# Optimization experiments

Measured on AMD Instinct MI355X. Metric: run time of the kernel, lower is better.

Reference implementation:

```python
import jax, jax.numpy as jnp
import numpy as np


def setup_inputs() -> dict:
    key = jax.random.key(0)
    k1, k2, k3, k4 = jax.random.split(key, 4)
    n, b, h, f = 8, 64, 128, 256
    hs = 64
    x = jax.random.normal(k1, (n, b, h, f), dtype=jnp.float32)
    # torch Linear weights are (out, in); store transposed as (in, out) for x @ W
    Wq = jax.random.normal(k2, (f, hs), dtype=jnp.float32) * (6.0 / (f + hs)) ** 0.5
    Wk = jax.random.normal(k3, (f, hs), dtype=jnp.float32) * (6.0 / (f + hs)) ** 0.5
    Wv = jax.random.normal(k4, (f, hs), dtype=jnp.float32) * (6.0 / (f + hs)) ** 0.5
    return {"x": x, "Wq": Wq, "Wk": Wk, "Wv": Wv}


def reference(x, Wq, Wk, Wv):
    # x: (n, b, h, f). NOTE: scale uses f = n_embd (as in the source), not head_size.
    f = x.shape[-1]
    scale = f ** (-0.5)
    Q = jnp.einsum('nbhf,fd->nbhd', x, Wq)  # (n, b, h, hs)
    K = jnp.einsum('nbhf,fd->nbhd', x, Wk)
    V = jnp.einsum('nbhf,fd->nbhd', x, Wv)
    # alphas[i, j, b, p, q] = sum_d Q[j,b,p,d] * K[i,b,q,d] * scale
    scores = jnp.einsum('jbpd,ibqd->ijbpq', Q, K) * scale  # (n, n, b, h, h)
    alphas = jax.nn.softmax(scores, axis=-1)
    # out[i, j, b, p, d] = sum_q alphas[i,j,b,p,q] V[i,b,q,d]; then sum over i
    o = jnp.einsum('ijbpq,ibqd->jbpd', alphas, V)  # (n, b, h, hs)
    return o
```

## Files before the change

### kernel.cpp

```cpp
#include <hip/hip_runtime.h>
#include <cstdint>

#define N_SEQ 8
#define B_DIM 64
#define H_DIM 128
#define F_DIM 256
#define HS 64

typedef __attribute__((ext_vector_type(8))) short short8;
typedef __attribute__((ext_vector_type(4))) float floatx4;

__device__ __forceinline__ ushort f2bf(float f) {
    union { float f; uint32_t u; } v; v.f = f;
    uint32_t r = v.u + 0x7FFF + ((v.u >> 16) & 1);
    return (ushort)(r >> 16);
}

__device__ __forceinline__ void async_ld16(const ushort* g, ushort* lds) {
    __builtin_amdgcn_global_load_lds(
        (const __attribute__((address_space(1))) unsigned int*)g,
        (__attribute__((address_space(3))) unsigned int*)lds,
        16, 0, 0);
}

__global__ __launch_bounds__(256) void prep_w(
    const float* __restrict__ Wq, const float* __restrict__ Wk,
    const float* __restrict__ Wv, ushort* __restrict__ Wtb)
{
    const int n = blockIdx.x;
    const float* W = (n < 64) ? Wq : (n < 128) ? Wk : Wv;
    const int c = n & 63;
    const int k = threadIdx.x;
    Wtb[n * 256 + k] = f2bf(W[k * 64 + c]);
}

#define XS_STRIDE 264
__global__ __launch_bounds__(256, 4) void proj_mfma(
    const float* __restrict__ x, const ushort* __restrict__ Wtb,
    ushort* __restrict__ Qb, ushort* __restrict__ Kb, ushort* __restrict__ Vtb)
{
    __shared__ ushort xs[64 * XS_STRIDE];
    const int t = threadIdx.x;
    const int blk = blockIdx.x;
    const int64_t row0 = (int64_t)blk * 64;

    const float4* xg = (const float4*)(x + row0 * F_DIM);
    #pragma unroll
    for (int u = 0; u < 8; ++u) {
        const int idx = t + 256 * u;
        const int row = idx >> 5;
        const int c8 = (idx & 31) * 8;
        const float4 a = xg[idx * 2];
        const float4 b = xg[idx * 2 + 1];
        *(ushort4*)&xs[row * XS_STRIDE + c8] =
            make_ushort4(f2bf(a.x), f2bf(a.y), f2bf(a.z), f2bf(a.w));
        *(ushort4*)&xs[row * XS_STRIDE + c8 + 4] =
            make_ushort4(f2bf(b.x), f2bf(b.y), f2bf(b.z), f2bf(b.w));
    }
    __syncthreads();

    const int w = t >> 6, lane = t & 63;
    const int q16 = lane >> 4, l16 = lane & 15;
    const int n0 = w * 48;

    floatx4 acc[4][3];
    #pragma unroll
    for (int mt = 0; mt < 4; ++mt)
        #pragma unroll
        for (int nt = 0; nt < 3; ++nt) acc[mt][nt] = (floatx4){0.f, 0.f, 0.f, 0.f};

    short8 nb[3];
    #pragma unroll
    for (int nt = 0; nt < 3; ++nt)
        nb[nt] = *(const short8*)&Wtb[(n0 + nt * 16 + l16) * 256 + q16 * 8];

    for (int ks = 0; ks < 8; ++ks) {
        short8 cur[3];
        #pragma unroll
        for (int nt = 0; nt < 3; ++nt) cur[nt] = nb[nt];
        if (ks < 7) {
            #pragma unroll
            for (int nt = 0; nt < 3; ++nt)
                nb[nt] = *(const short8*)&Wtb[(n0 + nt * 16 + l16) * 256 + (ks + 1) * 32 + q16 * 8];
        }
        #pragma unroll
        for (int mt = 0; mt < 4; ++mt) {
            const short8 afr = *(const short8*)&xs[(mt * 16 + l16) * XS_STRIDE + ks * 32 + q16 * 8];
            #pragma unroll
            for (int nt = 0; nt < 3; ++nt)
                acc[mt][nt] = __builtin_amdgcn_mfma_f32_16x16x32_bf16(afr, cur[nt], acc[mt][nt], 0, 0, 0);
        }
    }

    const float qscale = 0.0625f * 1.44269504f;
    #pragma unroll
    for (int mt = 0; mt < 4; ++mt) {
        const int64_t g = row0 + mt * 16 + q16 * 4;
        #pragma unroll
        for (int nt = 0; nt < 3; ++nt) {
            const int ntb = n0 + nt * 16;
            const int n = ntb + l16;
            if (ntb < 64) {
                #pragma unroll
                for (int r = 0; r < 4; ++r)
                    Qb[(g + r) * 64 + n] = f2bf(acc[mt][nt][r] * qscale);
            } else if (ntb < 128) {
                #pragma unroll
                for (int r = 0; r < 4; ++r)
                    Kb[(g + r) * 64 + (n - 64)] = f2bf(acc[mt][nt][r]);
            } else {
                const int d = n - 128;
                const int ib = (int)(g >> 7);
                const int h = (int)(g & 127);
                *(ushort4*)&Vtb[((int64_t)(ib * 64 + d)) * 128 + h] =
                    make_ushort4(f2bf(acc[mt][nt][0]), f2bf(acc[mt][nt][1]),
                                 f2bf(acc[mt][nt][2]), f2bf(acc[mt][nt][3]));
            }
        }
    }
}

#define PT_STRIDE 40
__global__ __launch_bounds__(256, 2) void attn_mfma(
    const ushort* __restrict__ Qb, const ushort* __restrict__ Kb,
    const ushort* __restrict__ Vtb, float* __restrict__ out)
{
    __shared__ ushort Ks[2][8192];
    __shared__ ushort Vt[2][8192];
    __shared__ ushort Ps[4][2][16 * PT_STRIDE];

    const int t = threadIdx.x;
    const int blk = blockIdx.x;
    const int b  = ((blk & 7) << 3) | ((blk >> 3) & 7);
    const int j  = blk >> 6;
    const int jb = j * 64 + b;

    const int w = t >> 6, lane = t & 63;
    const int q16 = lane >> 4, l16 = lane & 15;

    int koff[4], voff[4], ldsoff[4];
    #pragma unroll
    for (int u = 0; u < 4; ++u) {
        const int fi = w * 4 + u;
        koff[u] = ((fi & 7) * 16 + l16) * 64 + (fi >> 3) * 32 + q16 * 8;
        voff[u] = ((fi & 3) * 16 + l16) * 128 + (fi >> 2) * 32 + q16 * 8;
        ldsoff[u] = fi * 512;
    }

    const int prow = jb * H_DIM + w * 16 + l16;
    short8 qa[2][2];
    #pragma unroll
    for (int hh = 0; hh < 2; ++hh)
        #pragma unroll
        for (int ks = 0; ks < 2; ++ks)
            qa[hh][ks] = *(const short8*)&Qb[(prow + hh * 64) * 64 + ks * 32 + q16 * 8];

    floatx4 of[2][4];
    #pragma unroll
    for (int hh = 0; hh < 2; ++hh)
        #pragma unroll
        for (int mt = 0; mt < 4; ++mt) of[hh][mt] = (floatx4){0.f, 0.f, 0.f, 0.f};

    {
        const ushort* kg = Kb + ((0 * B_DIM + b) << 13);
        const ushort* vg = Vtb + ((0 * B_DIM + b) << 13);
        #pragma unroll
        for (int u = 0; u < 4; ++u) {
            const int lo = __builtin_amdgcn_readfirstlane(ldsoff[u]);
            async_ld16(kg + koff[u], &Ks[0][lo]);
            async_ld16(vg + voff[u], &Vt[0][lo]);
        }
    }

    for (int i = 0; i < N_SEQ; ++i) {
        const int buf = i & 1;
        __syncthreads();

        if (i < N_SEQ - 1) {
            const ushort* kg = Kb + (((i + 1) * B_DIM + b) << 13);
            const ushort* vg = Vtb + (((i + 1) * B_DIM + b) << 13);
            #pragma unroll
            for (int u = 0; u < 4; ++u) {
                const int lo = __builtin_amdgcn_readfirstlane(ldsoff[u]);
                async_ld16(kg + koff[u], &Ks[buf ^ 1][lo]);
                async_ld16(vg + voff[u], &Vt[buf ^ 1][lo]);
            }
        }

        floatx4 sf[2][8];
        #pragma unroll
        for (int hh = 0; hh < 2; ++hh)
            #pragma unroll
            for (int nt = 0; nt < 8; ++nt) sf[hh][nt] = (floatx4){0.f, 0.f, 0.f, 0.f};
        #pragma unroll
        for (int ks = 0; ks < 2; ++ks)
            #pragma unroll
            for (int nt = 0; nt < 8; ++nt) {
                const short8 ak = *(const short8*)&Ks[buf][(ks * 8 + nt) * 512 + lane * 8];
                sf[0][nt] = __builtin_amdgcn_mfma_f32_16x16x32_bf16(ak, qa[0][ks], sf[0][nt], 0, 0, 0);
                sf[1][nt] = __builtin_amdgcn_mfma_f32_16x16x32_bf16(ak, qa[1][ks], sf[1][nt], 0, 0, 0);
            }

        float inv[2];
        #pragma unroll
        for (int hh = 0; hh < 2; ++hh) {
            float l = 0.f;
            #pragma unroll
            for (int nt = 0; nt < 8; ++nt)
                #pragma unroll
                for (int r = 0; r < 4; ++r) {
                    sf[hh][nt][r] = __builtin_amdgcn_exp2f(sf[hh][nt][r]);
                    l += sf[hh][nt][r];
                }
            l += __shfl_xor(l, 16);
            l += __shfl_xor(l, 32);
            inv[hh] = __builtin_amdgcn_rcpf(l);
        }

        #pragma unroll
        for (int kq = 0; kq < 4; ++kq) {
            #pragma unroll
            for (int hh = 0; hh < 2; ++hh)
                #pragma unroll
                for (int tt = 0; tt < 2; ++tt) {
                    const int nt = kq * 2 + tt;
                    *(ushort4*)&Ps[w][hh][l16 * PT_STRIDE + tt * 16 + q16 * 4] =
                        make_ushort4(f2bf(sf[hh][nt][0] * inv[hh]),
                                     f2bf(sf[hh][nt][1] * inv[hh]),
                                     f2bf(sf[hh][nt][2] * inv[hh]),
                                     f2bf(sf[hh][nt][3] * inv[hh]));
                }
            const short8 bp0 = *(const short8*)&Ps[w][0][l16 * PT_STRIDE + q16 * 8];
            const short8 bp1 = *(const short8*)&Ps[w][1][l16 * PT_STRIDE + q16 * 8];
            #pragma unroll
            for (int mt = 0; mt < 4; ++mt) {
                const short8 av = *(const short8*)&Vt[buf][(kq * 4 + mt) * 512 + lane * 8];
                of[0][mt] = __builtin_amdgcn_mfma_f32_16x16x32_bf16(av, bp0, of[0][mt], 0, 0, 0);
                of[1][mt] = __builtin_amdgcn_mfma_f32_16x16x32_bf16(av, bp1, of[1][mt], 0, 0, 0);
            }
        }
    }

    #pragma unroll
    for (int hh = 0; hh < 2; ++hh)
        #pragma unroll
        for (int mt = 0; mt < 4; ++mt)
            *(float4*)&out[(int64_t)(prow + hh * 64) * HS + mt * 16 + q16 * 4] =
                make_float4(of[hh][mt][0], of[hh][mt][1], of[hh][mt][2], of[hh][mt][3]);
}

extern "C" void kernel_launch(void* const* d_in, const int* in_sizes, int n_in,
                              void* d_out, int out_size, void* d_ws, size_t ws_size,
                              hipStream_t stream)
{
    const float* x  = (const float*)d_in[0];
    const float* Wq = (const float*)d_in[1];
    const float* Wk = (const float*)d_in[2];
    const float* Wv = (const float*)d_in[3];
    float* out = (float*)d_out;

    const size_t qkv = (size_t)N_SEQ * B_DIM * H_DIM * HS;
    ushort* Qb  = (ushort*)d_ws;
    ushort* Kb  = Qb + qkv;
    ushort* Vtb = Kb + qkv;
    ushort* Wtb = Vtb + qkv;

    prep_w<<<192, 256, 0, stream>>>(Wq, Wk, Wv, Wtb);
    proj_mfma<<<(N_SEQ * B_DIM * H_DIM) / 64, 256, 0, stream>>>(x, Wtb, Qb, Kb, Vtb);
    attn_mfma<<<N_SEQ * B_DIM, 256, 0, stream>>>(Qb, Kb, Vtb, out);
}
```

Before: 148.3 us.

## Use 8 waves per attention block with half-tile K/V streaming and deferred normalization

The attention kernel moves from 4 waves each handling two 16-row query tiles to 8 waves each handling one tile, launched with 512 threads. K and V for each key block are now streamed in two 64-key halves through smaller double-buffered LDS tiles. Softmax normalization is deferred: unnormalized exp values go through PV, and the accumulator is scaled by the reciprocal row sum once per key block. This aims to raise occupancy and latency hiding through lower per-wave registers and LDS, at the cost of twice as many barriers and more frequent, smaller async loads.

```diff
diff --git a/kernel.cpp b/kernel.cpp
--- a/kernel.cpp
+++ b/kernel.cpp
@@ -121,13 +121,13 @@
 }
 
 #define PT_STRIDE 40
-__global__ __launch_bounds__(256, 2) void attn_mfma(
+__global__ __launch_bounds__(512, 4) void attn_mfma(
     const ushort* __restrict__ Qb, const ushort* __restrict__ Kb,
     const ushort* __restrict__ Vtb, float* __restrict__ out)
 {
-    __shared__ ushort Ks[2][8192];
-    __shared__ ushort Vt[2][8192];
-    __shared__ ushort Ps[4][2][16 * PT_STRIDE];
+    __shared__ ushort Ks[2][4096];
+    __shared__ ushort Vt[2][4096];
+    __shared__ ushort Ps[8][16 * PT_STRIDE];
 
     const int t = threadIdx.x;
     const int blk = blockIdx.x;
@@ -138,115 +138,98 @@
     const int w = t >> 6, lane = t & 63;
     const int q16 = lane >> 4, l16 = lane & 15;
 
-    int koff[4], voff[4], ldsoff[4];
-    #pragma unroll
-    for (int u = 0; u < 4; ++u) {
-        const int fi = w * 4 + u;
-        koff[u] = ((fi & 7) * 16 + l16) * 64 + (fi >> 3) * 32 + q16 * 8;
-        voff[u] = ((fi & 3) * 16 + l16) * 128 + (fi >> 2) * 32 + q16 * 8;
-        ldsoff[u] = fi * 512;
-    }
+    const int koff0 = ((w & 3) * 16 + l16) * 64 + (w >> 2) * 32 + q16 * 8;
+    const int voff0 = ((w & 3) * 16 + l16) * 128 + (w >> 2) * 32 + q16 * 8;
+    const int lo = __builtin_amdgcn_readfirstlane(w * 512);
 
     const int prow = jb * H_DIM + w * 16 + l16;
-    short8 qa[2][2];
-    #pragma unroll
-    for (int hh = 0; hh < 2; ++hh)
-        #pragma unroll
-        for (int ks = 0; ks < 2; ++ks)
-            qa[hh][ks] = *(const short8*)&Qb[(prow + hh * 64) * 64 + ks * 32 + q16 * 8];
-
-    floatx4 of[2][4];
-    #pragma unroll
-    for (int hh = 0; hh < 2; ++hh)
-        #pragma unroll
-        for (int mt = 0; mt < 4; ++mt) of[hh][mt] = (floatx4){0.f, 0.f, 0.f, 0.f};
+    short8 qa[2];
+    #pragma unroll
+    for (int ks = 0; ks < 2; ++ks)
+        qa[ks] = *(const short8*)&Qb[prow * 64 + ks * 32 + q16 * 8];
+
+    floatx4 of[4];
+    #pragma unroll
+    for (int mt = 0; mt < 4; ++mt) of[mt] = (floatx4){0.f, 0.f, 0.f, 0.f};
 
     {
         const ushort* kg = Kb + ((0 * B_DIM + b) << 13);
         const ushort* vg = Vtb + ((0 * B_DIM + b) << 13);
-        #pragma unroll
-        for (int u = 0; u < 4; ++u) {
-            const int lo = __builtin_amdgcn_readfirstlane(ldsoff[u]);
-            async_ld16(kg + koff[u], &Ks[0][lo]);
-            async_ld16(vg + voff[u], &Vt[0][lo]);
-        }
+        async_ld16(kg + koff0, &Ks[0][lo]);
+        async_ld16(vg + voff0, &Vt[0][lo]);
     }
 
     for (int i = 0; i < N_SEQ; ++i) {
-        const int buf = i & 1;
-        __syncthreads();
-
-        if (i < N_SEQ - 1) {
-            const ushort* kg = Kb + (((i + 1) * B_DIM + b) << 13);
-            const ushort* vg = Vtb + (((i + 1) * B_DIM + b) << 13);
-            #pragma unroll
-            for (int u = 0; u < 4; ++u) {
-                const int lo = __builtin_amdgcn_readfirstlane(ldsoff[u]);
-                async_ld16(kg + koff[u], &Ks[buf ^ 1][lo]);
-                async_ld16(vg + voff[u], &Vt[buf ^ 1][lo]);
+        float lsum = 0.f;
+        floatx4 tmp[4];
+        #pragma unroll
+        for (int mt = 0; mt < 4; ++mt) tmp[mt] = (floatx4){0.f, 0.f, 0.f, 0.f};
+
+        #pragma unroll
+        for (int s = 0; s < 2; ++s) {
+            const int step = i * 2 + s;
+            const int buf = step & 1;
+            __syncthreads();
+
+            if (step < 2 * N_SEQ - 1) {
+                const int i2 = (step + 1) >> 1, s2 = (step + 1) & 1;
+                const ushort* kg = Kb + ((i2 * B_DIM + b) << 13) + s2 * 4096;
+                const ushort* vg = Vtb + ((i2 * B_DIM + b) << 13) + s2 * 64;
+                async_ld16(kg + koff0, &Ks[buf ^ 1][lo]);
+                async_ld16(vg + voff0, &Vt[buf ^ 1][lo]);
             }
-        }
-
-        floatx4 sf[2][8];
-        #pragma unroll
-        for (int hh = 0; hh < 2; ++hh)
-            #pragma unroll
-            for (int nt = 0; nt < 8; ++nt) sf[hh][nt] = (floatx4){0.f, 0.f, 0.f, 0.f};
-        #pragma unroll
-        for (int ks = 0; ks < 2; ++ks)
-            #pragma unroll
-            for (int nt = 0; nt < 8; ++nt) {
-                const short8 ak = *(const short8*)&Ks[buf][(ks * 8 + nt) * 512 + lane * 8];
-                sf[0][nt] = __builtin_amdgcn_mfma_f32_16x16x32_bf16(ak, qa[0][ks], sf[0][nt], 0, 0, 0);
-                sf[1][nt] = __builtin_amdgcn_mfma_f32_16x16x32_bf16(ak, qa[1][ks], sf[1][nt], 0, 0, 0);
-            }
-
-        float inv[2];
-        #pragma unroll
-        for (int hh = 0; hh < 2; ++hh) {
-            float l = 0.f;
-            #pragma unroll
-            for (int nt = 0; nt < 8; ++nt)
+
+            floatx4 sf[4];
+            #pragma unroll
+            for (int nt = 0; nt < 4; ++nt) sf[nt] = (floatx4){0.f, 0.f, 0.f, 0.f};
+            #pragma unroll
+            for (int ks = 0; ks < 2; ++ks)
+                #pragma unroll
+                for (int nt = 0; nt < 4; ++nt) {
+                    const short8 ak = *(const short8*)&Ks[buf][(ks * 4 + nt) * 512 + lane * 8];
+                    sf[nt] = __builtin_amdgcn_mfma_f32_16x16x32_bf16(ak, qa[ks], sf[nt], 0, 0, 0);
+                }
+
+            #pragma unroll
+            for (int nt = 0; nt < 4; ++nt)
                 #pragma unroll
                 for (int r = 0; r < 4; ++r) {
-                    sf[hh][nt][r] = __builtin_amdgcn_exp2f(sf[hh][nt][r]);
-                    l += sf[hh][nt][r];
-                }
-            l += __shfl_xor(l, 16);
-            l += __shfl_xor(l, 32);
-            inv[hh] = __builtin_amdgcn_rcpf(l);
-        }
-
-        #pragma unroll
-        for (int kq = 0; kq < 4; ++kq) {
-            #pragma unroll
-            for (int hh = 0; hh < 2; ++hh)
+                    sf[nt][r] = __builtin_amdgcn_exp2f(sf[nt][r]);
+                    lsum += sf[nt][r];
+                }
+
+            #pragma unroll
+            for (int kq = 0; kq < 2; ++kq) {
                 #pragma unroll
                 for (int tt = 0; tt < 2; ++tt) {
                     const int nt = kq * 2 + tt;
-                    *(ushort4*)&Ps[w][hh][l16 * PT_STRIDE + tt * 16 + q16 * 4] =
-                        make_ushort4(f2bf(sf[hh][nt][0] * inv[hh]),
-                                     f2bf(sf[hh][nt][1] * inv[hh]),
-                                     f2bf(sf[hh][nt][2] * inv[hh]),
-                                     f2bf(sf[hh][nt][3] * inv[hh]));
-                }
-            const short8 bp0 = *(const short8*)&Ps[w][0][l16 * PT_STRIDE + q16 * 8];
-            const short8 bp1 = *(const short8*)&Ps[w][1][l16 * PT_STRIDE + q16 * 8];
-            #pragma unroll
-            for (int mt = 0; mt < 4; ++mt) {
-                const short8 av = *(const short8*)&Vt[buf][(kq * 4 + mt) * 512 + lane * 8];
-                of[0][mt] = __builtin_amdgcn_mfma_f32_16x16x32_bf16(av, bp0, of[0][mt], 0, 0, 0);
-                of[1][mt] = __builtin_amdgcn_mfma_f32_16x16x32_bf16(av, bp1, of[1][mt], 0, 0, 0);
+                    *(ushort4*)&Ps[w][l16 * PT_STRIDE + tt * 16 + q16 * 4] =
+                        make_ushort4(f2bf(sf[nt][0]), f2bf(sf[nt][1]),
+                                     f2bf(sf[nt][2]), f2bf(sf[nt][3]));
+                }
+                const short8 bp = *(const short8*)&Ps[w][l16 * PT_STRIDE + q16 * 8];
+                #pragma unroll
+                for (int mt = 0; mt < 4; ++mt) {
+                    const short8 av = *(const short8*)&Vt[buf][(kq * 4 + mt) * 512 + lane * 8];
+                    tmp[mt] = __builtin_amdgcn_mfma_f32_16x16x32_bf16(av, bp, tmp[mt], 0, 0, 0);
+                }
             }
         }
-    }
-
-    #pragma unroll
-    for (int hh = 0; hh < 2; ++hh)
+
+        lsum += __shfl_xor(lsum, 16);
+        lsum += __shfl_xor(lsum, 32);
+        const float inv = __builtin_amdgcn_rcpf(lsum);
         #pragma unroll
         for (int mt = 0; mt < 4; ++mt)
-            *(float4*)&out[(int64_t)(prow + hh * 64) * HS + mt * 16 + q16 * 4] =
-                make_float4(of[hh][mt][0], of[hh][mt][1], of[hh][mt][2], of[hh][mt][3]);
+            #pragma unroll
+            for (int r = 0; r < 4; ++r)
+                of[mt][r] += tmp[mt][r] * inv;
+    }
+
+    #pragma unroll
+    for (int mt = 0; mt < 4; ++mt)
+        *(float4*)&out[(int64_t)prow * HS + mt * 16 + q16 * 4] =
+            make_float4(of[mt][0], of[mt][1], of[mt][2], of[mt][3]);
 }
 
 extern "C" void kernel_launch(void* const* d_in, const int* in_sizes, int n_in,
@@ -267,5 +250,5 @@
 
     prep_w<<<192, 256, 0, stream>>>(Wq, Wk, Wv, Wtb);
     proj_mfma<<<(N_SEQ * B_DIM * H_DIM) / 64, 256, 0, stream>>>(x, Wtb, Qb, Kb, Vtb);
-    attn_mfma<<<N_SEQ * B_DIM, 256, 0, stream>>>(Qb, Kb, Vtb, out);
-}
+    attn_mfma<<<N_SEQ * B_DIM, 512, 0, stream>>>(Qb, Kb, Vtb, out);
+}
```

Measured after the change: 143.2 us, median of 2. 1.04x faster.
